# Kernel tuning notes

Measured on AMD Instinct MI355X. Metric: run time of the kernel, lower is better.

The kernel has to match this reference:

```python
import jax, jax.numpy as jnp
import numpy as np

NUM_HEADS = 8
ROPE_BASE = 10000.0

def rotate_half(x):
    x1, x2 = jnp.split(x, 2, axis=-1)
    return jnp.concatenate((-x2, x1), axis=-1)

def rope_cos_sin(seq_len, head_dim, dtype):
    inv_freq = 1.0 / (ROPE_BASE ** (jnp.arange(0, head_dim, 2, dtype=jnp.float32) / head_dim))
    t = jnp.arange(seq_len, dtype=jnp.float32)
    freqs = t[:, None] * inv_freq[None, :]            # [N, D/2]
    emb = jnp.concatenate((freqs, freqs), axis=-1)    # [N, D]
    cos = jnp.cos(emb)[None, None].astype(dtype)      # [1,1,N,D]
    sin = jnp.sin(emb)[None, None].astype(dtype)
    return cos, sin

def setup_inputs() -> dict:
    key = jax.random.key(0)
    k1, k2, k3 = jax.random.split(key, 3)
    B, N, C = 4, 2048, 512
    x = jax.random.normal(k1, (B, N, C), dtype=jnp.float32)
    w_qkv = jax.random.normal(k2, (C, 3 * C), dtype=jnp.float32) * (C ** -0.5)
    w_proj = jax.random.normal(k3, (C, C), dtype=jnp.float32) * (C ** -0.5)
    b_proj = jnp.zeros((C,), dtype=jnp.float32)
    return {"x": x, "w_qkv": w_qkv, "w_proj": w_proj, "b_proj": b_proj}

def reference(x, w_qkv, w_proj, b_proj):
    B, N, C = x.shape
    H = NUM_HEADS
    D = C // H
    scale = D ** -0.5
    qkv = (x @ w_qkv).reshape(B, N, 3, H, D).transpose(2, 0, 3, 1, 4)  # [3,B,H,N,D]
    q, k, v = qkv[0], qkv[1], qkv[2]
    cos, sin = rope_cos_sin(N, D, x.dtype)
    q = q * cos + rotate_half(q) * sin
    k = k * cos + rotate_half(k) * sin
    attn = jax.nn.softmax(jnp.einsum('bhnd,bhmd->bhnm', q, k) * scale, axis=-1)  # [B,H,N,N]
    out = jnp.einsum('bhnm,bhmd->bhnd', attn, v)      # [B,H,N,D]
    out = out.transpose(0, 2, 1, 3).reshape(B, N, C)
    out = out @ w_proj + b_proj
    return out, attn
```

## Files before the change

kernel.cpp:

```cpp
#include <hip/hip_runtime.h>
#include <math.h>


#define OFF_K 4194304
#define OFF_V 8388608

__global__ __launch_bounds__(256) void gemm_qkv_kernel(
    const float* __restrict__ x, const float* __restrict__ w,
    float* __restrict__ qb, float* __restrict__ kb, float* __restrict__ vb)
{
    __shared__ float As[8][132];
    __shared__ float Bs[8][132];
    const int tid  = threadIdx.x;
    const int row0 = blockIdx.x * 128;
    const int col0 = blockIdx.y * 128;
    const int tx = tid & 15, ty = tid >> 4;

    float acc[8][8];
    #pragma unroll
    for (int i = 0; i < 8; ++i)
        #pragma unroll
        for (int j = 0; j < 8; ++j) acc[i][j] = 0.0f;

    const int ar  = tid >> 1;
    const int ah  = (tid & 1) * 4;
    const int bkr = tid >> 5;
    const int bc  = (tid & 31) * 4;

    for (int k0 = 0; k0 < 512; k0 += 8) {
        float4 a4 = *(const float4*)(x + (size_t)(row0 + ar) * 512 + k0 + ah);
        float4 b4 = *(const float4*)(w + (size_t)(k0 + bkr) * 1536 + col0 + bc);
        __syncthreads();
        As[ah + 0][ar] = a4.x; As[ah + 1][ar] = a4.y;
        As[ah + 2][ar] = a4.z; As[ah + 3][ar] = a4.w;
        *(float4*)&Bs[bkr][bc] = b4;
        __syncthreads();
        #pragma unroll
        for (int kk = 0; kk < 8; ++kk) {
            float a[8], b[8];
            *(float4*)&a[0] = *(const float4*)&As[kk][ty * 8];
            *(float4*)&a[4] = *(const float4*)&As[kk][ty * 8 + 4];
            *(float4*)&b[0] = *(const float4*)&Bs[kk][tx * 8];
            *(float4*)&b[4] = *(const float4*)&Bs[kk][tx * 8 + 4];
            #pragma unroll
            for (int i = 0; i < 8; ++i)
                #pragma unroll
                for (int j = 0; j < 8; ++j)
                    acc[i][j] = fmaf(a[i], b[j], acc[i][j]);
        }
    }

    #pragma unroll
    for (int i = 0; i < 8; ++i) {
        int r  = row0 + ty * 8 + i;
        int b_ = r >> 11;
        int n  = r & 2047;
        #pragma unroll
        for (int j0 = 0; j0 < 8; j0 += 4) {
            int c     = col0 + tx * 8 + j0;
            int which = c >> 9;
            int h     = (c >> 6) & 7;
            int d     = c & 63;
            float* base = (which == 0) ? qb : ((which == 1) ? kb : vb);
            float* dst  = base + (((size_t)(b_ * 8 + h) * 2048 + n) * 64 + d);
            *(float4*)dst = make_float4(acc[i][j0], acc[i][j0 + 1],
                                        acc[i][j0 + 2], acc[i][j0 + 3]);
        }
    }
}

__global__ void rope_kernel(float* __restrict__ qb, float* __restrict__ kb)
{
    int idx = blockIdx.x * 256 + threadIdx.x;
    if (idx >= 4 * 8 * 2048 * 32) return;
    int i  = idx & 31;
    int n  = (idx >> 5) & 2047;
    int bh = idx >> 16;

    double invf = pow(10000.0, -(double)(2 * i) / 64.0);
    double ang  = (double)n * invf;
    float c = (float)cos(ang);
    float s = (float)sin(ang);

    size_t base = ((size_t)bh * 2048 + n) * 64;
    float q0 = qb[base + i], q1 = qb[base + i + 32];
    qb[base + i]      = q0 * c - q1 * s;
    qb[base + i + 32] = q1 * c + q0 * s;
    float k0 = kb[base + i], k1 = kb[base + i + 32];
    kb[base + i]      = k0 * c - k1 * s;
    kb[base + i + 32] = k1 * c + k0 * s;
}

__global__ __launch_bounds__(256) void attn_scores_kernel(
    const float* __restrict__ qb, const float* __restrict__ kb,
    float* __restrict__ attn)
{
    __shared__ float Qs[64][132];
    __shared__ float Ks[64][132];
    __shared__ float red[128][17];
    __shared__ float m_run[128], l_run[128];

    const int tid = threadIdx.x;
    const int bh  = blockIdx.x;
    const int n0  = blockIdx.y * 128;
    const int tx = tid & 15, ty = tid >> 4;

    const float* qbase = qb + ((size_t)bh * 2048 + n0) * 64;
    const float* kbase = kb + (size_t)bh * 2048 * 64;
    float* attn_base = attn + ((size_t)bh * 2048 + n0) * 2048;

    #pragma unroll
    for (int it = 0; it < 8; ++it) {
        int r = ty + it * 16;
        int d = tx * 4;
        float4 v4 = *(const float4*)(qbase + (size_t)r * 64 + d);
        Qs[d + 0][r] = v4.x; Qs[d + 1][r] = v4.y;
        Qs[d + 2][r] = v4.z; Qs[d + 3][r] = v4.w;
    }
    if (tid < 128) { m_run[tid] = -3.0e38f; l_run[tid] = 0.0f; }
    __syncthreads();

    for (int m0 = 0; m0 < 2048; m0 += 128) {
        float4 kv[8];
        #pragma unroll
        for (int it = 0; it < 8; ++it) {
            int c = ty + it * 16;
            kv[it] = *(const float4*)(kbase + (size_t)(m0 + c) * 64 + tx * 4);
        }
        __syncthreads();
        #pragma unroll
        for (int it = 0; it < 8; ++it) {
            int c = ty + it * 16;
            int d = tx * 4;
            Ks[d + 0][c] = kv[it].x; Ks[d + 1][c] = kv[it].y;
            Ks[d + 2][c] = kv[it].z; Ks[d + 3][c] = kv[it].w;
        }
        __syncthreads();

        float acc[8][8];
        #pragma unroll
        for (int i = 0; i < 8; ++i)
            #pragma unroll
            for (int j = 0; j < 8; ++j) acc[i][j] = 0.0f;

        #pragma unroll 4
        for (int d = 0; d < 64; ++d) {
            float a[8], b[8];
            *(float4*)&a[0] = *(const float4*)&Qs[d][ty * 8];
            *(float4*)&a[4] = *(const float4*)&Qs[d][ty * 8 + 4];
            *(float4*)&b[0] = *(const float4*)&Ks[d][tx * 8];
            *(float4*)&b[4] = *(const float4*)&Ks[d][tx * 8 + 4];
            #pragma unroll
            for (int i = 0; i < 8; ++i)
                #pragma unroll
                for (int j = 0; j < 8; ++j)
                    acc[i][j] = fmaf(a[i], b[j], acc[i][j]);
        }
        #pragma unroll
        for (int i = 0; i < 8; ++i)
            #pragma unroll
            for (int j = 0; j < 8; ++j) acc[i][j] *= 0.125f;

        #pragma unroll
        for (int i = 0; i < 8; ++i) {
            int r = ty * 8 + i;
            float* drow = attn_base + (size_t)r * 2048 + m0 + tx * 8;
            *(float4*)drow       = make_float4(acc[i][0], acc[i][1], acc[i][2], acc[i][3]);
            *(float4*)(drow + 4) = make_float4(acc[i][4], acc[i][5], acc[i][6], acc[i][7]);
        }

        #pragma unroll
        for (int i = 0; i < 8; ++i) {
            float mx = acc[i][0];
            #pragma unroll
            for (int j = 1; j < 8; ++j) mx = fmaxf(mx, acc[i][j]);
            red[ty * 8 + i][tx] = mx;
        }
        __syncthreads();
        if (tid < 128) {
            float tmax = red[tid][0];
            #pragma unroll
            for (int t = 1; t < 16; ++t) tmax = fmaxf(tmax, red[tid][t]);
            float m_old = m_run[tid];
            float m_new = fmaxf(m_old, tmax);
            l_run[tid] *= __expf(m_old - m_new);
            m_run[tid]  = m_new;
        }
        __syncthreads();
        #pragma unroll
        for (int i = 0; i < 8; ++i) {
            float mr = m_run[ty * 8 + i];
            float s = 0.0f;
            #pragma unroll
            for (int j = 0; j < 8; ++j) s += __expf(acc[i][j] - mr);
            red[ty * 8 + i][tx] = s;
        }
        __syncthreads();
        if (tid < 128) {
            float s = 0.0f;
            #pragma unroll
            for (int t = 0; t < 16; ++t) s += red[tid][t];
            l_run[tid] += s;
        }
    }
    __syncthreads();
    if (tid < 128) l_run[tid] = 1.0f / l_run[tid];
    __syncthreads();

    float4* arow = (float4*)attn_base;
    for (int idx = tid; idx < 128 * 512; idx += 256) {
        int r = idx >> 9;
        float m  = m_run[r];
        float li = l_run[r];
        float4 s4 = arow[idx];
        s4.x = __expf(s4.x - m) * li;
        s4.y = __expf(s4.y - m) * li;
        s4.z = __expf(s4.z - m) * li;
        s4.w = __expf(s4.w - m) * li;
        arow[idx] = s4;
    }
}

__global__ __launch_bounds__(128) void attn_pv_kernel(
    const float* __restrict__ attn, const float* __restrict__ vb,
    float* __restrict__ out_pre)
{
    __shared__ float As[16][132];
    __shared__ float Bs[16][68];
    const int tid = threadIdx.x;
    const int bh  = blockIdx.x;
    const int n0  = blockIdx.y * 128;
    const int b = bh >> 3, h = bh & 7;
    const int tx = tid & 7, ty = tid >> 3;

    const float* pbase = attn + ((size_t)bh * 2048 + n0) * 2048;
    const float* vbase = vb + (size_t)bh * 2048 * 64;

    float acc[8][8];
    #pragma unroll
    for (int i = 0; i < 8; ++i)
        #pragma unroll
        for (int j = 0; j < 8; ++j) acc[i][j] = 0.0f;

    const int ar  = tid >> 2;
    const int ahh = (tid & 3) * 4;
    const int vm  = tid >> 4;
    const int vd  = (tid & 15) * 4;

    for (int m0 = 0; m0 < 2048; m0 += 16) {
        float4 a4[4];
        #pragma unroll
        for (int it = 0; it < 4; ++it) {
            int r = ar + it * 32;
            a4[it] = *(const float4*)(pbase + (size_t)r * 2048 + m0 + ahh);
        }
        float4 b4[2];
        #pragma unroll
        for (int it = 0; it < 2; ++it) {
            int m = vm + it * 8;
            b4[it] = *(const float4*)(vbase + (size_t)(m0 + m) * 64 + vd);
        }
        __syncthreads();
        #pragma unroll
        for (int it = 0; it < 4; ++it) {
            int r = ar + it * 32;
            As[ahh + 0][r] = a4[it].x; As[ahh + 1][r] = a4[it].y;
            As[ahh + 2][r] = a4[it].z; As[ahh + 3][r] = a4[it].w;
        }
        #pragma unroll
        for (int it = 0; it < 2; ++it)
            *(float4*)&Bs[vm + it * 8][vd] = b4[it];
        __syncthreads();
        #pragma unroll 4
        for (int kk = 0; kk < 16; ++kk) {
            float a[8], bb[8];
            *(float4*)&a[0]  = *(const float4*)&As[kk][ty * 8];
            *(float4*)&a[4]  = *(const float4*)&As[kk][ty * 8 + 4];
            *(float4*)&bb[0] = *(const float4*)&Bs[kk][tx * 8];
            *(float4*)&bb[4] = *(const float4*)&Bs[kk][tx * 8 + 4];
            #pragma unroll
            for (int i = 0; i < 8; ++i)
                #pragma unroll
                for (int j = 0; j < 8; ++j)
                    acc[i][j] = fmaf(a[i], bb[j], acc[i][j]);
        }
    }

    #pragma unroll
    for (int i = 0; i < 8; ++i) {
        int n = n0 + ty * 8 + i;
        float* dst = out_pre + ((size_t)b * 2048 + n) * 512 + h * 64 + tx * 8;
        *(float4*)dst       = make_float4(acc[i][0], acc[i][1], acc[i][2], acc[i][3]);
        *(float4*)(dst + 4) = make_float4(acc[i][4], acc[i][5], acc[i][6], acc[i][7]);
    }
}

__global__ __launch_bounds__(256) void proj_kernel(
    const float* __restrict__ a, const float* __restrict__ w,
    const float* __restrict__ bias, float* __restrict__ out)
{
    __shared__ float As[8][132];
    __shared__ float Bs[8][132];
    const int tid  = threadIdx.x;
    const int row0 = blockIdx.x * 128;
    const int col0 = blockIdx.y * 128;
    const int tx = tid & 15, ty = tid >> 4;

    float acc[8][8];
    #pragma unroll
    for (int i = 0; i < 8; ++i)
        #pragma unroll
        for (int j = 0; j < 8; ++j) acc[i][j] = 0.0f;

    const int ar  = tid >> 1;
    const int ah  = (tid & 1) * 4;
    const int bkr = tid >> 5;
    const int bc  = (tid & 31) * 4;

    for (int k0 = 0; k0 < 512; k0 += 8) {
        float4 a4 = *(const float4*)(a + (size_t)(row0 + ar) * 512 + k0 + ah);
        float4 b4 = *(const float4*)(w + (size_t)(k0 + bkr) * 512 + col0 + bc);
        __syncthreads();
        As[ah + 0][ar] = a4.x; As[ah + 1][ar] = a4.y;
        As[ah + 2][ar] = a4.z; As[ah + 3][ar] = a4.w;
        *(float4*)&Bs[bkr][bc] = b4;
        __syncthreads();
        #pragma unroll
        for (int kk = 0; kk < 8; ++kk) {
            float av[8], bv[8];
            *(float4*)&av[0] = *(const float4*)&As[kk][ty * 8];
            *(float4*)&av[4] = *(const float4*)&As[kk][ty * 8 + 4];
            *(float4*)&bv[0] = *(const float4*)&Bs[kk][tx * 8];
            *(float4*)&bv[4] = *(const float4*)&Bs[kk][tx * 8 + 4];
            #pragma unroll
            for (int i = 0; i < 8; ++i)
                #pragma unroll
                for (int j = 0; j < 8; ++j)
                    acc[i][j] = fmaf(av[i], bv[j], acc[i][j]);
        }
    }

    float bj[8];
    #pragma unroll
    for (int j = 0; j < 8; ++j) bj[j] = bias[col0 + tx * 8 + j];

    #pragma unroll
    for (int i = 0; i < 8; ++i) {
        int r = row0 + ty * 8 + i;
        float* dst = out + (size_t)r * 512 + col0 + tx * 8;
        *(float4*)dst       = make_float4(acc[i][0] + bj[0], acc[i][1] + bj[1],
                                          acc[i][2] + bj[2], acc[i][3] + bj[3]);
        *(float4*)(dst + 4) = make_float4(acc[i][4] + bj[4], acc[i][5] + bj[5],
                                          acc[i][6] + bj[6], acc[i][7] + bj[7]);
    }
}

extern "C" void kernel_launch(void* const* d_in, const int* in_sizes, int n_in,
                              void* d_out, int out_size, void* d_ws, size_t ws_size,
                              hipStream_t stream)
{
    const float* x      = (const float*)d_in[0];
    const float* w_qkv  = (const float*)d_in[1];
    const float* w_proj = (const float*)d_in[2];
    const float* b_proj = (const float*)d_in[3];

    float* out  = (float*)d_out;
    float* attn = (float*)d_out + 4194304;

    float* ws = (float*)d_ws;
    float* q = ws;
    float* k = ws + OFF_K;
    float* v = ws + OFF_V;
    float* out_pre = ws;

    gemm_qkv_kernel<<<dim3(64, 12), 256, 0, stream>>>(x, w_qkv, q, k, v);
    rope_kernel<<<8192, 256, 0, stream>>>(q, k);
    attn_scores_kernel<<<dim3(32, 16), 256, 0, stream>>>(q, k, attn);
    attn_pv_kernel<<<dim3(32, 16), 128, 0, stream>>>(attn, v, out_pre);
    proj_kernel<<<dim3(64, 4), 256, 0, stream>>>(out_pre, w_proj, b_proj, out);
}
```

Measured before the change: 1.640 ms.

## Fuse attention scores, softmax and PV; add rope table, swizzled LDS, proj retile

Merges the scores/softmax kernel with the PV kernel. Per-tile exponentials are stored once with running max/sum kept in registers via warp shuffles, then rescaled by a per-tile correction factor while being reloaded for the PV product. This removes a full read-modify-write pass over the attention matrix and the separate PV read. RoPE cos/sin is precomputed into a table held in the attn buffer so the double-precision trig runs once per position instead of per head. LDS tiles now use an XOR swizzle in place of padding, the scale is folded into Q, and the projection kernel reads the head-major out_pre directly with smaller 64-row tiles. The gains come at the cost of more complex indexing and a workspace aliasing assumption.

```diff
diff --git a/kernel.cpp b/kernel.cpp
--- a/kernel.cpp
+++ b/kernel.cpp
@@ -4,6 +4,10 @@
 
 #define OFF_K 4194304
 #define OFF_V 8388608
+
+typedef float nf4 __attribute__((ext_vector_type(4)));
+
+#define SWZ(row, col) (((((col) >> 2) ^ (((row) >> 2) & 7)) << 2) | ((col) & 3))
 
 __global__ __launch_bounds__(256) void gemm_qkv_kernel(
     const float* __restrict__ x, const float* __restrict__ w,
@@ -69,7 +73,19 @@
     }
 }
 
-__global__ void rope_kernel(float* __restrict__ qb, float* __restrict__ kb)
+__global__ void rope_table_kernel(float2* __restrict__ tab)
+{
+    int idx = blockIdx.x * 256 + threadIdx.x;
+    if (idx >= 2048 * 32) return;
+    int i = idx & 31;
+    int n = idx >> 5;
+    double invf = pow(10000.0, -(double)(2 * i) / 64.0);
+    double ang  = (double)n * invf;
+    tab[idx] = make_float2((float)cos(ang), (float)sin(ang));
+}
+
+__global__ void rope_apply_kernel(float* __restrict__ qb, float* __restrict__ kb,
+                                  const float2* __restrict__ tab)
 {
     int idx = blockIdx.x * 256 + threadIdx.x;
     if (idx >= 4 * 8 * 2048 * 32) return;
@@ -77,10 +93,8 @@
     int n  = (idx >> 5) & 2047;
     int bh = idx >> 16;
 
-    double invf = pow(10000.0, -(double)(2 * i) / 64.0);
-    double ang  = (double)n * invf;
-    float c = (float)cos(ang);
-    float s = (float)sin(ang);
+    float2 cs = tab[(n << 5) | i];
+    float c = cs.x, s = cs.y;
 
     size_t base = ((size_t)bh * 2048 + n) * 64;
     float q0 = qb[base + i], q1 = qb[base + i + 32];
@@ -91,14 +105,18 @@
     kb[base + i + 32] = k1 * c + k0 * s;
 }
 
-__global__ __launch_bounds__(256) void attn_scores_kernel(
+__global__ __launch_bounds__(256) void attn_scores_pv_kernel(
     const float* __restrict__ qb, const float* __restrict__ kb,
-    float* __restrict__ attn)
-{
-    __shared__ float Qs[64][132];
-    __shared__ float Ks[64][132];
-    __shared__ float red[128][17];
-    __shared__ float m_run[128], l_run[128];
+    const float* __restrict__ vb, float* __restrict__ attn,
+    float* __restrict__ out_pre)
+{
+    __shared__ float smem[18560];
+    float (*Qs)[128] = (float (*)[128])smem;
+    float (*Ks)[128] = (float (*)[128])(smem + 8192);
+    float (*Ps)[128] = (float (*)[128])smem;
+    float (*Vs)[68]  = (float (*)[68])(smem + 8192);
+    float (*mt)[16]  = (float (*)[16])(smem + 16384);
+    float* l_lds     = smem + 18432;
 
     const int tid = threadIdx.x;
     const int bh  = blockIdx.x;
@@ -107,6 +125,7 @@
 
     const float* qbase = qb + ((size_t)bh * 2048 + n0) * 64;
     const float* kbase = kb + (size_t)bh * 2048 * 64;
+    const float* vbase = vb + (size_t)bh * 2048 * 64;
     float* attn_base = attn + ((size_t)bh * 2048 + n0) * 2048;
 
     #pragma unroll
@@ -114,10 +133,13 @@
         int r = ty + it * 16;
         int d = tx * 4;
         float4 v4 = *(const float4*)(qbase + (size_t)r * 64 + d);
-        Qs[d + 0][r] = v4.x; Qs[d + 1][r] = v4.y;
-        Qs[d + 2][r] = v4.z; Qs[d + 3][r] = v4.w;
-    }
-    if (tid < 128) { m_run[tid] = -3.0e38f; l_run[tid] = 0.0f; }
+        int pc = SWZ(d, r);
+        Qs[d + 0][pc] = v4.x * 0.125f; Qs[d + 1][pc] = v4.y * 0.125f;
+        Qs[d + 2][pc] = v4.z * 0.125f; Qs[d + 3][pc] = v4.w * 0.125f;
+    }
+    float m[8], l[8];
+    #pragma unroll
+    for (int i = 0; i < 8; ++i) { m[i] = -3.0e38f; l[i] = 0.0f; }
     __syncthreads();
 
     for (int m0 = 0; m0 < 2048; m0 += 128) {
@@ -132,8 +154,9 @@
         for (int it = 0; it < 8; ++it) {
             int c = ty + it * 16;
             int d = tx * 4;
-            Ks[d + 0][c] = kv[it].x; Ks[d + 1][c] = kv[it].y;
-            Ks[d + 2][c] = kv[it].z; Ks[d + 3][c] = kv[it].w;
+            int pc = SWZ(d, c);
+            Ks[d + 0][pc] = kv[it].x; Ks[d + 1][pc] = kv[it].y;
+            Ks[d + 2][pc] = kv[it].z; Ks[d + 3][pc] = kv[it].w;
         }
         __syncthreads();
 
@@ -145,21 +168,43 @@
 
         #pragma unroll 4
         for (int d = 0; d < 64; ++d) {
+            const int sk = (d >> 2) & 7;
             float a[8], b[8];
-            *(float4*)&a[0] = *(const float4*)&Qs[d][ty * 8];
-            *(float4*)&a[4] = *(const float4*)&Qs[d][ty * 8 + 4];
-            *(float4*)&b[0] = *(const float4*)&Ks[d][tx * 8];
-            *(float4*)&b[4] = *(const float4*)&Ks[d][tx * 8 + 4];
+            *(float4*)&a[0] = *(const float4*)&Qs[d][((ty * 2 + 0) ^ sk) << 2];
+            *(float4*)&a[4] = *(const float4*)&Qs[d][((ty * 2 + 1) ^ sk) << 2];
+            *(float4*)&b[0] = *(const float4*)&Ks[d][((tx * 2 + 0) ^ sk) << 2];
+            *(float4*)&b[4] = *(const float4*)&Ks[d][((tx * 2 + 1) ^ sk) << 2];
             #pragma unroll
             for (int i = 0; i < 8; ++i)
                 #pragma unroll
                 for (int j = 0; j < 8; ++j)
                     acc[i][j] = fmaf(a[i], b[j], acc[i][j]);
         }
-        #pragma unroll
-        for (int i = 0; i < 8; ++i)
-            #pragma unroll
-            for (int j = 0; j < 8; ++j) acc[i][j] *= 0.125f;
+
+        #pragma unroll
+        for (int i = 0; i < 8; ++i) {
+            float mx = acc[i][0];
+            #pragma unroll
+            for (int j = 1; j < 8; ++j) mx = fmaxf(mx, acc[i][j]);
+            mx = fmaxf(mx, __shfl_xor(mx, 1));
+            mx = fmaxf(mx, __shfl_xor(mx, 2));
+            mx = fmaxf(mx, __shfl_xor(mx, 4));
+            mx = fmaxf(mx, __shfl_xor(mx, 8));
+            float mn = fmaxf(m[i], mx);
+            l[i] *= __expf(m[i] - mn);
+            m[i]  = mn;
+            float s = 0.0f;
+            #pragma unroll
+            for (int j = 0; j < 8; ++j) {
+                acc[i][j] = __expf(acc[i][j] - mn);
+                s += acc[i][j];
+            }
+            s += __shfl_xor(s, 1);
+            s += __shfl_xor(s, 2);
+            s += __shfl_xor(s, 4);
+            s += __shfl_xor(s, 8);
+            l[i] += s;
+        }
 
         #pragma unroll
         for (int i = 0; i < 8; ++i) {
@@ -168,130 +213,91 @@
             *(float4*)drow       = make_float4(acc[i][0], acc[i][1], acc[i][2], acc[i][3]);
             *(float4*)(drow + 4) = make_float4(acc[i][4], acc[i][5], acc[i][6], acc[i][7]);
         }
-
-        #pragma unroll
-        for (int i = 0; i < 8; ++i) {
-            float mx = acc[i][0];
-            #pragma unroll
-            for (int j = 1; j < 8; ++j) mx = fmaxf(mx, acc[i][j]);
-            red[ty * 8 + i][tx] = mx;
-        }
-        __syncthreads();
-        if (tid < 128) {
-            float tmax = red[tid][0];
-            #pragma unroll
-            for (int t = 1; t < 16; ++t) tmax = fmaxf(tmax, red[tid][t]);
-            float m_old = m_run[tid];
-            float m_new = fmaxf(m_old, tmax);
-            l_run[tid] *= __expf(m_old - m_new);
-            m_run[tid]  = m_new;
-        }
-        __syncthreads();
-        #pragma unroll
-        for (int i = 0; i < 8; ++i) {
-            float mr = m_run[ty * 8 + i];
-            float s = 0.0f;
-            #pragma unroll
-            for (int j = 0; j < 8; ++j) s += __expf(acc[i][j] - mr);
-            red[ty * 8 + i][tx] = s;
-        }
-        __syncthreads();
-        if (tid < 128) {
-            float s = 0.0f;
-            #pragma unroll
-            for (int t = 0; t < 16; ++t) s += red[tid][t];
-            l_run[tid] += s;
-        }
+        if (tx == 0) {
+            int t = m0 >> 7;
+            #pragma unroll
+            for (int i = 0; i < 8; ++i) mt[ty * 8 + i][t] = m[i];
+        }
+    }
+    if (tx == 0) {
+        #pragma unroll
+        for (int i = 0; i < 8; ++i) l_lds[ty * 8 + i] = l[i];
     }
     __syncthreads();
-    if (tid < 128) l_run[tid] = 1.0f / l_run[tid];
+
+    {
+        int r  = tid >> 1;
+        int c0 = (tid & 1) * 8;
+        float v[8];
+        #pragma unroll
+        for (int j = 0; j < 8; ++j) v[j] = mt[r][c0 + j];
+        float mf = mt[r][15];
+        float lv = l_lds[r];
+        __syncthreads();
+        #pragma unroll
+        for (int j = 0; j < 8; ++j) mt[r][c0 + j] = __expf(v[j] - mf) / lv;
+    }
     __syncthreads();
 
-    float4* arow = (float4*)attn_base;
-    for (int idx = tid; idx < 128 * 512; idx += 256) {
-        int r = idx >> 9;
-        float m  = m_run[r];
-        float li = l_run[r];
-        float4 s4 = arow[idx];
-        s4.x = __expf(s4.x - m) * li;
-        s4.y = __expf(s4.y - m) * li;
-        s4.z = __expf(s4.z - m) * li;
-        s4.w = __expf(s4.w - m) * li;
-        arow[idx] = s4;
-    }
-}
-
-__global__ __launch_bounds__(128) void attn_pv_kernel(
-    const float* __restrict__ attn, const float* __restrict__ vb,
-    float* __restrict__ out_pre)
-{
-    __shared__ float As[16][132];
-    __shared__ float Bs[16][68];
-    const int tid = threadIdx.x;
-    const int bh  = blockIdx.x;
-    const int n0  = blockIdx.y * 128;
-    const int b = bh >> 3, h = bh & 7;
-    const int tx = tid & 7, ty = tid >> 3;
-
-    const float* pbase = attn + ((size_t)bh * 2048 + n0) * 2048;
-    const float* vbase = vb + (size_t)bh * 2048 * 64;
-
-    float acc[8][8];
+    float accO[8][4];
     #pragma unroll
     for (int i = 0; i < 8; ++i)
         #pragma unroll
-        for (int j = 0; j < 8; ++j) acc[i][j] = 0.0f;
-
-    const int ar  = tid >> 2;
-    const int ahh = (tid & 3) * 4;
-    const int vm  = tid >> 4;
-    const int vd  = (tid & 15) * 4;
-
-    for (int m0 = 0; m0 < 2048; m0 += 16) {
-        float4 a4[4];
-        #pragma unroll
-        for (int it = 0; it < 4; ++it) {
-            int r = ar + it * 32;
-            a4[it] = *(const float4*)(pbase + (size_t)r * 2048 + m0 + ahh);
-        }
-        float4 b4[2];
-        #pragma unroll
-        for (int it = 0; it < 2; ++it) {
-            int m = vm + it * 8;
-            b4[it] = *(const float4*)(vbase + (size_t)(m0 + m) * 64 + vd);
-        }
-        __syncthreads();
-        #pragma unroll
-        for (int it = 0; it < 4; ++it) {
-            int r = ar + it * 32;
-            As[ahh + 0][r] = a4[it].x; As[ahh + 1][r] = a4[it].y;
-            As[ahh + 2][r] = a4[it].z; As[ahh + 3][r] = a4[it].w;
-        }
-        #pragma unroll
-        for (int it = 0; it < 2; ++it)
-            *(float4*)&Bs[vm + it * 8][vd] = b4[it];
-        __syncthreads();
+        for (int j = 0; j < 4; ++j) accO[i][j] = 0.0f;
+
+    for (int s0 = 0; s0 < 2048; s0 += 64) {
+        const int t = s0 >> 7;
+        float4 vv[4];
+        #pragma unroll
+        for (int it = 0; it < 4; ++it)
+            vv[it] = *(const float4*)(vbase + (size_t)(s0 + ty + it * 16) * 64 + tx * 4);
+
+        float4 pp[8];
+        #pragma unroll
+        for (int it = 0; it < 8; ++it) {
+            int r = ty + it * 16;
+            float c = mt[r][t];
+            float* prow = attn_base + (size_t)r * 2048 + s0 + tx * 4;
+            float4 s4 = *(const float4*)prow;
+            s4.x *= c; s4.y *= c; s4.z *= c; s4.w *= c;
+            pp[it] = s4;
+            nf4 nt = { s4.x, s4.y, s4.z, s4.w };
+            __builtin_nontemporal_store(nt, (nf4*)prow);
+        }
+
+        __syncthreads();
+        #pragma unroll
+        for (int it = 0; it < 4; ++it)
+            *(float4*)&Vs[ty + it * 16][tx * 4] = vv[it];
+        #pragma unroll
+        for (int it = 0; it < 8; ++it) {
+            int r = ty + it * 16;
+            int mcol = tx * 4;
+            int pc = SWZ(mcol, r);
+            Ps[mcol + 0][pc] = pp[it].x; Ps[mcol + 1][pc] = pp[it].y;
+            Ps[mcol + 2][pc] = pp[it].z; Ps[mcol + 3][pc] = pp[it].w;
+        }
+        __syncthreads();
+
         #pragma unroll 4
-        for (int kk = 0; kk < 16; ++kk) {
-            float a[8], bb[8];
-            *(float4*)&a[0]  = *(const float4*)&As[kk][ty * 8];
-            *(float4*)&a[4]  = *(const float4*)&As[kk][ty * 8 + 4];
-            *(float4*)&bb[0] = *(const float4*)&Bs[kk][tx * 8];
-            *(float4*)&bb[4] = *(const float4*)&Bs[kk][tx * 8 + 4];
+        for (int kk = 0; kk < 64; ++kk) {
+            const int sk = (kk >> 2) & 7;
+            float a[8], b[4];
+            *(float4*)&a[0] = *(const float4*)&Ps[kk][((ty * 2 + 0) ^ sk) << 2];
+            *(float4*)&a[4] = *(const float4*)&Ps[kk][((ty * 2 + 1) ^ sk) << 2];
+            *(float4*)&b[0] = *(const float4*)&Vs[kk][tx * 4];
             #pragma unroll
             for (int i = 0; i < 8; ++i)
                 #pragma unroll
-                for (int j = 0; j < 8; ++j)
-                    acc[i][j] = fmaf(a[i], bb[j], acc[i][j]);
+                for (int j = 0; j < 4; ++j)
+                    accO[i][j] = fmaf(a[i], b[j], accO[i][j]);
         }
     }
 
     #pragma unroll
     for (int i = 0; i < 8; ++i) {
-        int n = n0 + ty * 8 + i;
-        float* dst = out_pre + ((size_t)b * 2048 + n) * 512 + h * 64 + tx * 8;
-        *(float4*)dst       = make_float4(acc[i][0], acc[i][1], acc[i][2], acc[i][3]);
-        *(float4*)(dst + 4) = make_float4(acc[i][4], acc[i][5], acc[i][6], acc[i][7]);
+        float* dst = out_pre + ((size_t)bh * 2048 + n0 + ty * 8 + i) * 64 + tx * 4;
+        *(float4*)dst = make_float4(accO[i][0], accO[i][1], accO[i][2], accO[i][3]);
     }
 }
 
@@ -299,59 +305,68 @@
     const float* __restrict__ a, const float* __restrict__ w,
     const float* __restrict__ bias, float* __restrict__ out)
 {
-    __shared__ float As[8][132];
+    __shared__ float As[8][68];
     __shared__ float Bs[8][132];
     const int tid  = threadIdx.x;
-    const int row0 = blockIdx.x * 128;
+    const int row0 = blockIdx.x * 64;
     const int col0 = blockIdx.y * 128;
-    const int tx = tid & 15, ty = tid >> 4;
-
-    float acc[8][8];
+    const int tx = tid & 31, ty = tid >> 5;
+
+    float acc[8][4];
     #pragma unroll
     for (int i = 0; i < 8; ++i)
         #pragma unroll
-        for (int j = 0; j < 8; ++j) acc[i][j] = 0.0f;
+        for (int j = 0; j < 4; ++j) acc[i][j] = 0.0f;
 
     const int ar  = tid >> 1;
     const int ah  = (tid & 1) * 4;
     const int bkr = tid >> 5;
     const int bc  = (tid & 31) * 4;
 
+    const int r_  = row0 + ar;
+    const int b_  = r_ >> 11;
+    const int n_  = r_ & 2047;
+
     for (int k0 = 0; k0 < 512; k0 += 8) {
-        float4 a4 = *(const float4*)(a + (size_t)(row0 + ar) * 512 + k0 + ah);
+        float4 a4;
+        if (tid < 128) {
+            const int kk_ = k0 + ah;
+            const int h_  = kk_ >> 6;
+            const int d_  = kk_ & 63;
+            a4 = *(const float4*)(a + (((size_t)(b_ * 8 + h_) * 2048 + n_) * 64 + d_));
+        }
         float4 b4 = *(const float4*)(w + (size_t)(k0 + bkr) * 512 + col0 + bc);
         __syncthreads();
-        As[ah + 0][ar] = a4.x; As[ah + 1][ar] = a4.y;
-        As[ah + 2][ar] = a4.z; As[ah + 3][ar] = a4.w;
+        if (tid < 128) {
+            As[ah + 0][ar] = a4.x; As[ah + 1][ar] = a4.y;
+            As[ah + 2][ar] = a4.z; As[ah + 3][ar] = a4.w;
+        }
         *(float4*)&Bs[bkr][bc] = b4;
         __syncthreads();
         #pragma unroll
         for (int kk = 0; kk < 8; ++kk) {
-            float av[8], bv[8];
+            float av[8], bv[4];
             *(float4*)&av[0] = *(const float4*)&As[kk][ty * 8];
             *(float4*)&av[4] = *(const float4*)&As[kk][ty * 8 + 4];
-            *(float4*)&bv[0] = *(const float4*)&Bs[kk][tx * 8];
-            *(float4*)&bv[4] = *(const float4*)&Bs[kk][tx * 8 + 4];
+            *(float4*)&bv[0] = *(const float4*)&Bs[kk][tx * 4];
             #pragma unroll
             for (int i = 0; i < 8; ++i)
                 #pragma unroll
-                for (int j = 0; j < 8; ++j)
+                for (int j = 0; j < 4; ++j)
                     acc[i][j] = fmaf(av[i], bv[j], acc[i][j]);
         }
     }
 
-    float bj[8];
-    #pragma unroll
-    for (int j = 0; j < 8; ++j) bj[j] = bias[col0 + tx * 8 + j];
+    float bj[4];
+    #pragma unroll
+    for (int j = 0; j < 4; ++j) bj[j] = bias[col0 + tx * 4 + j];
 
     #pragma unroll
     for (int i = 0; i < 8; ++i) {
         int r = row0 + ty * 8 + i;
-        float* dst = out + (size_t)r * 512 + col0 + tx * 8;
-        *(float4*)dst       = make_float4(acc[i][0] + bj[0], acc[i][1] + bj[1],
-                                          acc[i][2] + bj[2], acc[i][3] + bj[3]);
-        *(float4*)(dst + 4) = make_float4(acc[i][4] + bj[4], acc[i][5] + bj[5],
-                                          acc[i][6] + bj[6], acc[i][7] + bj[7]);
+        float* dst = out + (size_t)r * 512 + col0 + tx * 4;
+        *(float4*)dst = make_float4(acc[i][0] + bj[0], acc[i][1] + bj[1],
+                                    acc[i][2] + bj[2], acc[i][3] + bj[3]);
     }
 }
 
@@ -373,9 +388,11 @@
     float* v = ws + OFF_V;
     float* out_pre = ws;
 
+    float2* rope_tab = (float2*)attn;
+
     gemm_qkv_kernel<<<dim3(64, 12), 256, 0, stream>>>(x, w_qkv, q, k, v);
-    rope_kernel<<<8192, 256, 0, stream>>>(q, k);
-    attn_scores_kernel<<<dim3(32, 16), 256, 0, stream>>>(q, k, attn);
-    attn_pv_kernel<<<dim3(32, 16), 128, 0, stream>>>(attn, v, out_pre);
-    proj_kernel<<<dim3(64, 4), 256, 0, stream>>>(out_pre, w_proj, b_proj, out);
-}
+    rope_table_kernel<<<256, 256, 0, stream>>>(rope_tab);
+    rope_apply_kernel<<<8192, 256, 0, stream>>>(q, k, rope_tab);
+    attn_scores_pv_kernel<<<dim3(32, 16), 256, 0, stream>>>(q, k, v, attn, out_pre);
+    proj_kernel<<<dim3(128, 4), 256, 0, stream>>>(out_pre, w_proj, b_proj, out);
+}
```

After: 1.312 ms. -20.0%, faster.
